# Performance work log

Hardware: AMD Instinct MI355X
Metric: run time of the kernel (lower is better)

## Reference

```python
import jax, jax.numpy as jnp
import numpy as np

B, T, C, H, S = 4, 1024, 768, 12, 64  # batch, seq, emb_dim, n_heads, head_size
FF = 4 * C          # 3072, ff_hidden_size (required by SwiGLU input dim)
HID = int(8 * C / 3)  # 2048, SwiGLU hidden
EPS = 1e-6


def _rope_tables(seq_len, dim):
    # theta = 10000 ** (-2 * arange(0, dim, 2) / dim)  (note extra factor 2 vs standard RoPE)
    theta = 10000.0 ** (-2.0 * jnp.arange(0, dim, 2, dtype=jnp.float32) / dim)
    freqs = jnp.arange(seq_len, dtype=jnp.float32)[:, None] * theta  # [T, dim/2]
    cos = jnp.repeat(jnp.cos(freqs), 2, axis=-1)  # [T, dim]
    sin = jnp.repeat(jnp.sin(freqs), 2, axis=-1)
    return cos, sin


def _rope(x, cos, sin):
    # x: [..., T, S]; rotate pairs: even' = -odd, odd' = even
    rot = jnp.stack([-x[..., 1::2], x[..., 0::2]], axis=-1).reshape(x.shape)
    return x * cos + rot * sin


def _rmsnorm(x, gamma):
    # global scalar RMS over the whole tensor (faithful to torch.mean with no dim)
    return x / jnp.sqrt(EPS + jnp.mean(x * x)) * gamma


def _block(x, Wq, Wk, Wv, Wo, g1, g2, W1, b1, Ww, bw, Wg, bg, Wd, bd, W2, b2):
    Tlen = x.shape[1]
    cos, sin = _rope_tables(Tlen, S)
    # --- multi-head attention on rms1(x) ---
    h = _rmsnorm(x, g1)
    q = jnp.einsum('btc,hcs->bhts', h, Wq)
    k = jnp.einsum('btc,hcs->bhts', h, Wk)
    v = jnp.einsum('btc,hcs->bhts', h, Wv)
    rq = _rope(q, cos, sin)
    rk = _rope(k, cos, sin)
    scores = jnp.einsum('bhts,bhks->bhtk', rq, rk) * (C ** -0.5)  # scale by emb_dim, faithful
    causal = jnp.tril(jnp.ones((Tlen, Tlen), dtype=bool))
    scores = jnp.where(causal, scores, -jnp.inf)
    probs = jax.nn.softmax(scores, axis=-1)
    attn = jnp.einsum('bhtk,bhks->bhts', probs, v)
    attn = attn.transpose(0, 2, 1, 3).reshape(x.shape[0], Tlen, C)  # concat heads
    out = x + attn @ Wo
    # --- feed forward on rms2(out) ---
    h2 = _rmsnorm(out, g2)
    u = h2 @ W1 + b1                      # [B,T,FF]
    wx = u @ Ww + bw                      # [B,T,HID]
    vx = u @ Wg + bg
    ff = (wx * (vx * jax.nn.sigmoid(vx))) @ Wd + bd  # [B,T,FF]
    ff = ff @ W2 + b2                     # [B,T,C]
    return out + ff


def setup_inputs() -> dict:
    key = jax.random.key(0)
    ks = jax.random.split(key, 17)
    sd = 0.02
    return {
        'x':  jax.random.normal(ks[0], (B, T, C), jnp.float32),
        'Wq': jax.random.normal(ks[1], (H, C, S), jnp.float32) * sd,
        'Wk': jax.random.normal(ks[2], (H, C, S), jnp.float32) * sd,
        'Wv': jax.random.normal(ks[3], (H, C, S), jnp.float32) * sd,
        'Wo': jax.random.normal(ks[4], (C, C), jnp.float32) * sd,
        'g1': jnp.ones((C,), jnp.float32),
        'g2': jnp.ones((C,), jnp.float32),
        'W1': jax.random.normal(ks[5], (C, FF), jnp.float32) * sd,
        'b1': jnp.zeros((FF,), jnp.float32),
        'Ww': jax.random.normal(ks[6], (FF, HID), jnp.float32) * sd,
        'bw': jnp.zeros((HID,), jnp.float32),
        'Wg': jax.random.normal(ks[7], (FF, HID), jnp.float32) * sd,
        'bg': jnp.zeros((HID,), jnp.float32),
        'Wd': jax.random.normal(ks[8], (HID, FF), jnp.float32) * sd,
        'bd': jnp.zeros((FF,), jnp.float32),
        'W2': jax.random.normal(ks[9], (FF, C), jnp.float32) * sd,
        'b2': jnp.zeros((C,), jnp.float32),
    }


def reference(x, Wq, Wk, Wv, Wo, g1, g2, W1, b1, Ww, bw, Wg, bg, Wd, bd, W2, b2):
    return _block(x, Wq, Wk, Wv, Wo, g1, g2, W1, b1, Ww, bw, Wg, bg, Wd, bd, W2, b2)
```

## Files before the change

kernel.cpp:

```cpp
#include <hip/hip_runtime.h>
#include <math.h>

#define BB   4
#define TT   1024
#define CC   768
#define HH   12
#define SS   64
#define FFD  3072
#define HIDD 2048
#define NTOK (BB*TT)
#define EPSR 1e-6f

typedef __attribute__((ext_vector_type(8))) short bf16x8;
typedef __attribute__((ext_vector_type(4))) float f32x4;

__device__ __forceinline__ unsigned short f2bf(float f) {
    unsigned u = __float_as_uint(f);
    return (unsigned short)((u + 0x7FFFu + ((u >> 16) & 1u)) >> 16);
}
__device__ __forceinline__ float bfl(unsigned u) { return __uint_as_float(u << 16); }
__device__ __forceinline__ float bfh(unsigned u) { return __uint_as_float(u & 0xFFFF0000u); }
__device__ __forceinline__ unsigned pk2(float a, float b) {
    return (unsigned)f2bf(a) | ((unsigned)f2bf(b) << 16);
}

__device__ __forceinline__ void gload_lds16(const unsigned short* g, unsigned short* l) {
    __builtin_amdgcn_global_load_lds(
        (const __attribute__((address_space(1))) unsigned int*)g,
        (__attribute__((address_space(3))) unsigned int*)l, 16, 0, 0);
}

__global__ void k_scale_gamma_b(const float* __restrict__ x, const float* __restrict__ g,
                                const float* __restrict__ part, unsigned short* __restrict__ h,
                                int n8, float invn, int npart) {
    __shared__ float sm[256];
    float s = 0.f;
    for (int i = threadIdx.x; i < npart; i += 256) s += part[i];
    sm[threadIdx.x] = s;
    __syncthreads();
    for (int off = 128; off > 0; off >>= 1) {
        if (threadIdx.x < off) sm[threadIdx.x] += sm[threadIdx.x + off];
        __syncthreads();
    }
    float sc = 1.0f / sqrtf(EPSR + sm[0] * invn);
    int i = blockIdx.x * blockDim.x + threadIdx.x;
    if (i >= n8) return;
    float4 v0 = ((const float4*)x)[2*i];
    float4 v1 = ((const float4*)x)[2*i+1];
    int c = (i * 8) % CC;
    float4 g0 = *(const float4*)(g + c);
    float4 g1v = *(const float4*)(g + c + 4);
    uint4 r;
    r.x = pk2(v0.x*sc*g0.x,  v0.y*sc*g0.y);
    r.y = pk2(v0.z*sc*g0.z,  v0.w*sc*g0.w);
    r.z = pk2(v1.x*sc*g1v.x, v1.y*sc*g1v.y);
    r.w = pk2(v1.z*sc*g1v.z, v1.w*sc*g1v.w);
    ((uint4*)h)[i] = r;
}

#define TQKV 1728
#define TWO  576
#define TW1  2304
#define TWW  6144
#define TWD  6144
#define TW2  2304
#define J0 (TQKV)
#define J1 (J0 + TWO)
#define J2 (J1 + TW1)
#define J3 (J2 + TWW)
#define J4 (J3 + TWW)
#define J5 (J4 + TWD)
#define J6 (J5 + TW2)
#define J7 (J6 + 16)
#define J8 (J7 + 128)
#define JSUM 1024
#define J9 (J8 + JSUM)

__device__ __forceinline__ void wT_tile(float (*tl)[33], const float* __restrict__ W,
                                        unsigned short* __restrict__ Wt,
                                        int K, int N, int t, int tx, int ty) {
    int nk = K >> 5;
    int k0 = (t % nk) * 32, n0 = (t / nk) * 32;
#pragma unroll
    for (int i = 0; i < 4; ++i)
        tl[ty + i*8][tx] = W[(size_t)(k0 + ty + i*8) * N + n0 + tx];
    __syncthreads();
#pragma unroll
    for (int i = 0; i < 4; ++i)
        Wt[(size_t)(n0 + ty + i*8) * K + k0 + tx] = f2bf(tl[tx][ty + i*8]);
}

__global__ void k_prep(const float* __restrict__ Wq, const float* __restrict__ Wk,
                       const float* __restrict__ Wv, const float* __restrict__ Wo,
                       const float* __restrict__ W1, const float* __restrict__ Ww,
                       const float* __restrict__ Wg, const float* __restrict__ Wd,
                       const float* __restrict__ W2, const float* __restrict__ bw,
                       const float* __restrict__ bg, const float* __restrict__ x,
                       unsigned short* __restrict__ wqkvT, unsigned short* __restrict__ WoT,
                       unsigned short* __restrict__ W1T, unsigned short* __restrict__ WcatT,
                       unsigned short* __restrict__ WdT, unsigned short* __restrict__ W2T,
                       float* __restrict__ bcat, float* __restrict__ tab,
                       float* __restrict__ part) {
    __shared__ float tl[32][33];
    const int bid = blockIdx.x;
    const int tx = threadIdx.x & 31, ty = threadIdx.x >> 5;
    if (bid < J0) {
        int t = bid;
        int c0 = (t % 24) * 32;
        int s0 = ((t / 24) & 1) * 32;
        int z = t / 48, sel = z / HH, h = z % HH;
        const float* W = (sel == 0 ? Wq : (sel == 1 ? Wk : Wv)) + (size_t)h * CC * SS;
#pragma unroll
        for (int i = 0; i < 4; ++i)
            tl[ty + i*8][tx] = W[(size_t)(c0 + ty + i*8) * SS + s0 + tx];
        __syncthreads();
#pragma unroll
        for (int i = 0; i < 4; ++i)
            wqkvT[(size_t)(sel*CC + h*SS + s0 + ty + i*8) * CC + c0 + tx] = f2bf(tl[tx][ty + i*8]);
    } else if (bid < J1) {
        wT_tile(tl, Wo, WoT, CC, CC, bid - J0, tx, ty);
    } else if (bid < J2) {
        wT_tile(tl, W1, W1T, CC, FFD, bid - J1, tx, ty);
    } else if (bid < J3) {
        wT_tile(tl, Ww, WcatT, FFD, HIDD, bid - J2, tx, ty);
    } else if (bid < J4) {
        wT_tile(tl, Wg, WcatT + (size_t)HIDD*FFD, FFD, HIDD, bid - J3, tx, ty);
    } else if (bid < J5) {
        wT_tile(tl, Wd, WdT, HIDD, FFD, bid - J4, tx, ty);
    } else if (bid < J6) {
        wT_tile(tl, W2, W2T, FFD, CC, bid - J5, tx, ty);
    } else if (bid < J7) {
        int i = (bid - J6) * 256 + threadIdx.x;
        bcat[i] = (i < HIDD) ? bw[i] : bg[i - HIDD];
    } else if (bid < J8) {
        int i = (bid - J7) * 256 + threadIdx.x;
        int t = i >> 5, j = i & 31;
        float th = expf(-(float)j * 0.5756462732485115f);
        float ang = (float)t * th;
        tab[2*i]   = cosf(ang);
        tab[2*i+1] = sinf(ang);
    } else {
        float* sm = &tl[0][0];
        const int pb = bid - J8;
        const int n4 = NTOK * CC / 4;
        float s = 0.f;
        int stride = JSUM * 256;
        for (int i = pb * 256 + threadIdx.x; i < n4; i += stride) {
            float4 v = ((const float4*)x)[i];
            s += v.x*v.x + v.y*v.y + v.z*v.z + v.w*v.w;
        }
        sm[threadIdx.x] = s;
        __syncthreads();
        for (int off = 128; off > 0; off >>= 1) {
            if (threadIdx.x < off) sm[threadIdx.x] += sm[threadIdx.x + off];
            __syncthreads();
        }
        if (threadIdx.x == 0) part[pb] = sm[0];
    }
}

__global__ void k_rope_vt(unsigned short* __restrict__ qkv, const float* __restrict__ tab,
                          unsigned short* __restrict__ vtg) {
    const int bid = blockIdx.x;
    if (bid < 6144) {
        int i = bid * 256 + threadIdx.x;
        int j  = i & 31;
        int h  = (i >> 5) % HH;
        int bt = i / (32 * HH);
        int t  = bt & (TT - 1);
        float cs = tab[(t*32 + j)*2];
        float sn = tab[(t*32 + j)*2 + 1];
        size_t base = (size_t)bt * (3*CC) + h * SS + 2*j;
        unsigned q = *(unsigned*)(qkv + base);
        float qe = bfl(q), qo = bfh(q);
        *(unsigned*)(qkv + base) = pk2(qe*cs - qo*sn, qo*cs + qe*sn);
        unsigned k = *(unsigned*)(qkv + base + CC);
        float ke = bfl(k), ko = bfh(k);
        *(unsigned*)(qkv + base + CC) = pk2(ke*cs - ko*sn, ko*cs + ke*sn);
    } else {
        int b2 = bid - 6144;
        int bh = b2 >> 3, ty = b2 & 7;
        int b = bh / HH, h = bh % HH;
        int d = threadIdx.x & 63, tq = threadIdx.x >> 6;
        int t0 = ty * 128 + tq * 32;
        const unsigned short* src = qkv + (size_t)(b*TT + t0)*(3*CC) + 2*CC + h*SS + d;
        unsigned v[16];
#pragma unroll
        for (int e = 0; e < 16; ++e) {
            unsigned lo = src[(size_t)(2*e)*(3*CC)];
            unsigned hi = src[(size_t)(2*e+1)*(3*CC)];
            v[e] = (lo & 0xFFFFu) | (hi << 16);
        }
        uint4* dst = (uint4*)(vtg + ((size_t)bh*64 + d)*TT + t0);
#pragma unroll
        for (int q = 0; q < 4; ++q)
            dst[q] = make_uint4(v[q*4], v[q*4+1], v[q*4+2], v[q*4+3]);
    }
}

template<bool BIAS, bool RES, bool OUTB, bool SSQ>
__global__ __launch_bounds__(256) void k_gemm_bf16(
    const unsigned short* __restrict__ A, const unsigned short* __restrict__ Bt,
    const float* __restrict__ bias, const float* __restrict__ res,
    void* __restrict__ Cv, int M, int N, int K, float* __restrict__ ssq_part)
{
    __shared__ unsigned short As[2][128*32];
    __shared__ unsigned short Bs[2][128*32];
    __shared__ float smr[256];
    const int tid  = threadIdx.x;
    const int w    = tid >> 6, lane = tid & 63;
    const int wr   = w >> 1,  wc   = w & 1;
    const int row0 = blockIdx.y * 128, col0 = blockIdx.x * 128;

    f32x4 acc[4][4];
#pragma unroll
    for (int m = 0; m < 4; ++m)
#pragma unroll
        for (int n = 0; n < 4; ++n) acc[m][n] = (f32x4){0.f, 0.f, 0.f, 0.f};

    const int lr4 = lane >> 2;
    const int scb = lane & 3;

    auto stage = [&](int t, int buf) {
#pragma unroll
        for (int i = 0; i < 2; ++i) {
            int lr = w * 32 + i * 16 + lr4;
            int cbs = scb ^ ((lr >> 1) & 3);
            const unsigned short* ga = A + (size_t)(row0 + lr) * K + t * 32 + cbs * 8;
            gload_lds16(ga, &As[buf][(w * 32 + i * 16) * 32]);
            const unsigned short* gb = Bt + (size_t)(col0 + lr) * K + t * 32 + cbs * 8;
            gload_lds16(gb, &Bs[buf][(w * 32 + i * 16) * 32]);
        }
    };

    const int nt = K / 32;
    stage(0, 0);
    int cur = 0;
    const int fr = lane & 15, fq = lane >> 4;
    for (int t = 0; t < nt; ++t) {
        __syncthreads();
        if (t + 1 < nt) stage(t + 1, cur ^ 1);
        bf16x8 af[4], bf[4];
#pragma unroll
        for (int m = 0; m < 4; ++m) {
            int ra = wr * 64 + m * 16 + fr;
            af[m] = *(const bf16x8*)&As[cur][ra * 32 + (fq ^ ((ra >> 1) & 3)) * 8];
            int rb = wc * 64 + m * 16 + fr;
            bf[m] = *(const bf16x8*)&Bs[cur][rb * 32 + (fq ^ ((rb >> 1) & 3)) * 8];
        }
#pragma unroll
        for (int m = 0; m < 4; ++m)
#pragma unroll
            for (int n = 0; n < 4; ++n)
                acc[m][n] = __builtin_amdgcn_mfma_f32_16x16x32_bf16(af[m], bf[n], acc[m][n], 0, 0, 0);
        cur ^= 1;
    }

    float ssq = 0.f;
#pragma unroll
    for (int m = 0; m < 4; ++m) {
#pragma unroll
        for (int n = 0; n < 4; ++n) {
            int col = col0 + wc * 64 + n * 16 + fr;
            float bv = BIAS ? bias[col] : 0.f;
#pragma unroll
            for (int j = 0; j < 4; ++j) {
                int row = row0 + wr * 64 + m * 16 + fq * 4 + j;
                size_t off = (size_t)row * N + col;
                float v = acc[m][n][j] + bv;
                if (RES) v += res[off];
                if (OUTB) ((unsigned short*)Cv)[off] = f2bf(v);
                else      ((float*)Cv)[off] = v;
                if (SSQ) ssq += v * v;
            }
        }
    }
    if (SSQ) {
        smr[tid] = ssq;
        __syncthreads();
        for (int off = 128; off > 0; off >>= 1) {
            if (tid < off) smr[tid] += smr[tid + off];
            __syncthreads();
        }
        if (tid == 0) ssq_part[blockIdx.y * gridDim.x + blockIdx.x] = smr[0];
    }
}

#define INTERVAL(s_, RA, RB, NA, NB, DOSTAGE, DONEXT, LGKM, GATE)                 \
    {                                                                             \
        if (DONEXT) {                                                             \
            const int nx_ = ((s_) + 1) & 3;                                       \
            _Pragma("unroll")                                                     \
            for (int m = 0; m < 8; ++m)                                           \
                NA[m] = *(const bf16x8*)&ringA[nx_][offA[m]];                     \
            _Pragma("unroll")                                                     \
            for (int n = 0; n < 4; ++n)                                           \
                NB[n] = *(const bf16x8*)&ringB[nx_][offB[n]];                     \
        }                                                                         \
        if (DOSTAGE) { stageA((s_) + 3); stageB((s_) + 3); }                      \
        __builtin_amdgcn_sched_barrier(0);                                        \
        asm volatile("s_waitcnt " LGKM ::: "memory");                             \
        __builtin_amdgcn_sched_barrier(0);                                        \
        __builtin_amdgcn_s_setprio(1);                                            \
        _Pragma("unroll")                                                         \
        for (int m = 0; m < 8; ++m)                                               \
            _Pragma("unroll")                                                     \
            for (int n = 0; n < 4; ++n)                                           \
                acc[m][n] = __builtin_amdgcn_mfma_f32_16x16x32_bf16(              \
                    RA[m], RB[n], acc[m][n], 0, 0, 0);                            \
        __builtin_amdgcn_s_setprio(0);                                            \
        asm volatile("s_waitcnt " GATE ::: "memory");                             \
        __builtin_amdgcn_sched_barrier(0);                                        \
        __builtin_amdgcn_s_barrier();                                             \
    }

template<bool BIAS>
__global__ __launch_bounds__(512, 2) void k_gemm256(
    const unsigned short* __restrict__ A, const unsigned short* __restrict__ Bt,
    const float* __restrict__ bias, unsigned short* __restrict__ C,
    int M, int N, int K)
{
    __shared__ __align__(16) unsigned short ringA[4][256*32];
    __shared__ __align__(16) unsigned short ringB[4][256*32];
    const int tid = threadIdx.x;
    const int w = tid >> 6, lane = tid & 63;
    const int wm = w >> 2, wn = w & 3;
    const int fr = lane & 15, fq = lane >> 4;

    const int nwg = gridDim.x * gridDim.y;
    const int bid = blockIdx.y * gridDim.x + blockIdx.x;
    const int cpx = nwg >> 3;
    const int sbid = (bid & 7) * cpx + (bid >> 3);
    const int row0 = (sbid / gridDim.x) * 256;
    const int col0 = (sbid % gridDim.x) * 256;

    f32x4 acc[8][4];
#pragma unroll
    for (int m = 0; m < 8; ++m)
#pragma unroll
        for (int n = 0; n < 4; ++n) acc[m][n] = (f32x4){0.f, 0.f, 0.f, 0.f};

    const int c0 = tid, c1 = 512 + tid;
    const int r0 = c0 >> 2, p0 = ((c0 & 3) ^ ((r0 >> 1) & 3)) * 8;
    const int r1 = c1 >> 2, p1 = ((c1 & 3) ^ ((r1 >> 1) & 3)) * 8;
    const unsigned short* aS0 = A  + (size_t)(row0 + r0) * K + p0;
    const unsigned short* aS1 = A  + (size_t)(row0 + r1) * K + p1;
    const unsigned short* bS0 = Bt + (size_t)(col0 + r0) * K + p0;
    const unsigned short* bS1 = Bt + (size_t)(col0 + r1) * K + p1;
    const int dL = w * 512;
    auto stageA = [&](int t) {
        const int st = t & 3;
        const int kb = t * 32;
        gload_lds16(aS0 + kb, &ringA[st][dL]);
        gload_lds16(aS1 + kb, &ringA[st][4096 + dL]);
    };
    auto stageB = [&](int t) {
        const int st = t & 3;
        const int kb = t * 32;
        gload_lds16(bS0 + kb, &ringB[st][dL]);
        gload_lds16(bS1 + kb, &ringB[st][4096 + dL]);
    };

    int offA[8], offB[4];
#pragma unroll
    for (int m = 0; m < 8; ++m) {
        int ra = wm*128 + m*16 + fr;
        offA[m] = ra*32 + (fq ^ ((ra >> 1) & 3))*8;
    }
#pragma unroll
    for (int n = 0; n < 4; ++n) {
        int rb = wn*64 + n*16 + fr;
        offB[n] = rb*32 + (fq ^ ((rb >> 1) & 3))*8;
    }

    const int S = K >> 5;
    stageA(0); stageB(0); stageA(1); stageB(1); stageA(2); stageB(2);
    asm volatile("s_waitcnt vmcnt(4)" ::: "memory");
    __builtin_amdgcn_s_barrier();

    bf16x8 A0[8], B0[4], A1[8], B1[4];
#pragma unroll
    for (int m = 0; m < 8; ++m) A0[m] = *(const bf16x8*)&ringA[0][offA[m]];
#pragma unroll
    for (int n = 0; n < 4; ++n) B0[n] = *(const bf16x8*)&ringB[0][offB[n]];

    int s = 0;
    for (; s < S - 4; s += 2) {
        INTERVAL(s,   A0, B0, A1, B1, true, true, "lgkmcnt(12)", "vmcnt(4)");
        INTERVAL(s+1, A1, B1, A0, B0, true, true, "lgkmcnt(12)", "vmcnt(4)");
    }
    INTERVAL(S-4, A0, B0, A1, B1, true,  true,  "lgkmcnt(12)", "vmcnt(4)");
    INTERVAL(S-3, A1, B1, A0, B0, false, true,  "lgkmcnt(12)", "vmcnt(0)");
    INTERVAL(S-2, A0, B0, A1, B1, false, true,  "lgkmcnt(12)", "vmcnt(0)");
    INTERVAL(S-1, A1, B1, A0, B0, false, false, "lgkmcnt(0)",  "vmcnt(0)");

#pragma unroll
    for (int m = 0; m < 8; ++m) {
#pragma unroll
        for (int n = 0; n < 4; ++n) {
            int col = col0 + wn*64 + n*16 + fr;
            float bvb = BIAS ? bias[col] : 0.f;
#pragma unroll
            for (int j = 0; j < 4; ++j) {
                int row = row0 + wm*128 + m*16 + fq*4 + j;
                C[(size_t)row * N + col] = f2bf(acc[m][n][j] + bvb);
            }
        }
    }
}

__global__ __launch_bounds__(256) void k_attn_mfma(
    const unsigned short* __restrict__ qkv, const unsigned short* __restrict__ vtg,
    unsigned short* __restrict__ attn)
{
    __shared__ __align__(16) unsigned short Ks[2][64*64];
    __shared__ __align__(16) unsigned short Vs[2][64*64];
    __shared__ __align__(16) unsigned short Ps[4][16*72];
    const int tid = threadIdx.x;
    const int w = tid >> 6, lane = tid & 63;
    const int fr = lane & 15, fq = lane >> 4;
    const int bh = blockIdx.x, b = bh / HH, h = bh % HH;
    const int qb = blockIdx.y * 64;
    const int nkt = qb / 64 + 1;
    const float scale = 0.03608439182435161f;

    bf16x8 qf[2];
    {
        const unsigned short* qp = qkv + (size_t)(b*TT + qb + w*16 + fr)*(3*CC) + h*SS + fq*8;
        qf[0] = *(const bf16x8*)qp;
        qf[1] = *(const bf16x8*)(qp + 32);
    }

    auto stage = [&](int kt, int buf) {
        const unsigned short* kbase = qkv + (size_t)(b*TT + kt*64)*(3*CC) + CC + h*SS;
        const unsigned short* vbase = vtg + ((size_t)bh*64)*TT + kt*64;
#pragma unroll
        for (int p = 0; p < 2; ++p) {
            int s = p*256 + tid;
            int row = s >> 3;
            int blk = (s & 7) ^ (row & 7);
            gload_lds16(kbase + (size_t)row*(3*CC) + blk*8, &Ks[buf][(p*256 + w*64)*8]);
            gload_lds16(vbase + (size_t)row*TT + blk*8,     &Vs[buf][(p*256 + w*64)*8]);
        }
    };

    float m[4] = {-INFINITY, -INFINITY, -INFINITY, -INFINITY};
    float l[4] = {0.f, 0.f, 0.f, 0.f};
    f32x4 oacc[4];
#pragma unroll
    for (int n = 0; n < 4; ++n) oacc[n] = (f32x4){0.f, 0.f, 0.f, 0.f};

    stage(0, 0);
    int cur = 0;
    for (int kt = 0; kt < nkt; ++kt) {
        __syncthreads();
        if (kt + 1 < nkt) stage(kt + 1, cur ^ 1);

        f32x4 sacc[4];
#pragma unroll
        for (int n = 0; n < 4; ++n) sacc[n] = (f32x4){0.f, 0.f, 0.f, 0.f};
#pragma unroll
        for (int ks = 0; ks < 2; ++ks) {
#pragma unroll
            for (int n = 0; n < 4; ++n) {
                int row = n*16 + fr;
                bf16x8 kf = *(const bf16x8*)&Ks[cur][row*64 + ((ks*4 + fq) ^ (row & 7))*8];
                sacc[n] = __builtin_amdgcn_mfma_f32_16x16x32_bf16(qf[ks], kf, sacc[n], 0, 0, 0);
            }
        }

        float sv[4][4];
        const bool lastt = (kt == nkt - 1);
        const int qloc = w*16 + fq*4;
#pragma unroll
        for (int n = 0; n < 4; ++n) {
            int kloc = n*16 + fr;
#pragma unroll
            for (int j = 0; j < 4; ++j) {
                float vv = sacc[n][j] * scale;
                if (lastt && kloc > qloc + j) vv = -INFINITY;
                sv[j][n] = vv;
            }
        }
        float mx[4], ls[4];
#pragma unroll
        for (int j = 0; j < 4; ++j)
            mx[j] = fmaxf(fmaxf(sv[j][0], sv[j][1]), fmaxf(sv[j][2], sv[j][3]));
#pragma unroll
        for (int d = 1; d < 16; d <<= 1)
#pragma unroll
            for (int j = 0; j < 4; ++j) mx[j] = fmaxf(mx[j], __shfl_xor(mx[j], d));
        float corr[4];
#pragma unroll
        for (int j = 0; j < 4; ++j) {
            float nm = fmaxf(m[j], mx[j]);
            corr[j] = __expf(m[j] - nm);
            m[j] = nm;
        }
#pragma unroll
        for (int j = 0; j < 4; ++j) {
            float s0 = 0.f;
#pragma unroll
            for (int n = 0; n < 4; ++n) {
                float p = __expf(sv[j][n] - m[j]);
                sv[j][n] = p;
                s0 += p;
            }
            ls[j] = s0;
        }
#pragma unroll
        for (int d = 1; d < 16; d <<= 1)
#pragma unroll
            for (int j = 0; j < 4; ++j) ls[j] += __shfl_xor(ls[j], d);
#pragma unroll
        for (int j = 0; j < 4; ++j) l[j] = l[j]*corr[j] + ls[j];
#pragma unroll
        for (int n = 0; n < 4; ++n)
#pragma unroll
            for (int j = 0; j < 4; ++j) oacc[n][j] *= corr[j];

#pragma unroll
        for (int j = 0; j < 4; ++j)
#pragma unroll
            for (int n = 0; n < 4; ++n)
                Ps[w][(fq*4 + j)*72 + n*16 + fr] = f2bf(sv[j][n]);

#pragma unroll
        for (int ks = 0; ks < 2; ++ks) {
            bf16x8 pf = *(const bf16x8*)&Ps[w][fr*72 + ks*32 + fq*8];
#pragma unroll
            for (int n = 0; n < 4; ++n) {
                int row = n*16 + fr;
                bf16x8 vf = *(const bf16x8*)&Vs[cur][row*64 + ((ks*4 + fq) ^ (row & 7))*8];
                oacc[n] = __builtin_amdgcn_mfma_f32_16x16x32_bf16(pf, vf, oacc[n], 0, 0, 0);
            }
        }
        cur ^= 1;
    }

    float inv[4];
#pragma unroll
    for (int j = 0; j < 4; ++j) inv[j] = 1.0f / l[j];
#pragma unroll
    for (int n = 0; n < 4; ++n)
#pragma unroll
        for (int j = 0; j < 4; ++j) {
            size_t off = (size_t)(b*TT + qb + w*16 + fq*4 + j)*CC + h*SS + n*16 + fr;
            attn[off] = f2bf(oacc[n][j] * inv[j]);
        }
}

__global__ void k_swiglu_uv(const unsigned short* __restrict__ uv,
                            unsigned short* __restrict__ sw, int n8) {
    int i = blockIdx.x * blockDim.x + threadIdx.x;
    if (i >= n8) return;
    int r = i >> 8;
    int c8 = (i & 255) * 8;
    uint4 wv = *(const uint4*)(uv + (size_t)r * (2*HIDD) + c8);
    uint4 vv = *(const uint4*)(uv + (size_t)r * (2*HIDD) + HIDD + c8);
    uint4 rr;
    float w0, w1, v0, v1;
    w0 = bfl(wv.x); w1 = bfh(wv.x); v0 = bfl(vv.x); v1 = bfh(vv.x);
    rr.x = pk2(w0*v0/(1.f+__expf(-v0)), w1*v1/(1.f+__expf(-v1)));
    w0 = bfl(wv.y); w1 = bfh(wv.y); v0 = bfl(vv.y); v1 = bfh(vv.y);
    rr.y = pk2(w0*v0/(1.f+__expf(-v0)), w1*v1/(1.f+__expf(-v1)));
    w0 = bfl(wv.z); w1 = bfh(wv.z); v0 = bfl(vv.z); v1 = bfh(vv.z);
    rr.z = pk2(w0*v0/(1.f+__expf(-v0)), w1*v1/(1.f+__expf(-v1)));
    w0 = bfl(wv.w); w1 = bfh(wv.w); v0 = bfl(vv.w); v1 = bfh(vv.w);
    rr.w = pk2(w0*v0/(1.f+__expf(-v0)), w1*v1/(1.f+__expf(-v1)));
    *(uint4*)(sw + (size_t)r * HIDD + c8) = rr;
}

extern "C" void kernel_launch(void* const* d_in, const int* in_sizes, int n_in,
                              void* d_out, int out_size, void* d_ws, size_t ws_size,
                              hipStream_t stream)
{
    const float* x  = (const float*)d_in[0];
    const float* Wq = (const float*)d_in[1];
    const float* Wk = (const float*)d_in[2];
    const float* Wv = (const float*)d_in[3];
    const float* Wo = (const float*)d_in[4];
    const float* g1 = (const float*)d_in[5];
    const float* g2 = (const float*)d_in[6];
    const float* W1 = (const float*)d_in[7];
    const float* b1 = (const float*)d_in[8];
    const float* Ww = (const float*)d_in[9];
    const float* bw = (const float*)d_in[10];
    const float* Wg = (const float*)d_in[11];
    const float* bg = (const float*)d_in[12];
    const float* Wd = (const float*)d_in[13];
    const float* bd = (const float*)d_in[14];
    const float* W2 = (const float*)d_in[15];
    const float* b2 = (const float*)d_in[16];
    float* out = (float*)d_out;

    char* p = (char*)d_ws;
    auto alloc = [&](size_t bytes) { char* r = p; p += (bytes + 255) & ~(size_t)255; return r; };

    float*          part   = (float*)alloc(4096);
    float*          tab    = (float*)alloc((size_t)TT*32*2*4);
    float*          bcat   = (float*)alloc((size_t)2*HIDD*4);
    unsigned short* hb     = (unsigned short*)alloc((size_t)NTOK*CC*2);
    unsigned short* wqkvT  = (unsigned short*)alloc((size_t)3*CC*CC*2);
    unsigned short* qkvb   = (unsigned short*)alloc((size_t)NTOK*3*CC*2);
    unsigned short* vtg    = (unsigned short*)alloc((size_t)BB*HH*SS*TT*2);
    unsigned short* attnb  = (unsigned short*)alloc((size_t)NTOK*CC*2);
    unsigned short* WoT    = (unsigned short*)alloc((size_t)CC*CC*2);
    unsigned short* W1T    = (unsigned short*)alloc((size_t)FFD*CC*2);
    unsigned short* ub     = (unsigned short*)alloc((size_t)NTOK*FFD*2);
    unsigned short* WcatT  = (unsigned short*)alloc((size_t)2*HIDD*FFD*2);
    unsigned short* uvcat  = (unsigned short*)alloc((size_t)NTOK*2*HIDD*2);
    unsigned short* swb    = (unsigned short*)alloc((size_t)NTOK*HIDD*2);
    unsigned short* WdT    = (unsigned short*)alloc((size_t)FFD*HIDD*2);
    unsigned short* W2T    = (unsigned short*)alloc((size_t)CC*FFD*2);

    const int n = NTOK * CC;

    k_prep<<<J9, 256, 0, stream>>>(Wq, Wk, Wv, Wo, W1, Ww, Wg, Wd, W2, bw, bg, x,
                                   wqkvT, WoT, W1T, WcatT, WdT, W2T, bcat, tab, part);

    k_scale_gamma_b<<<(n/8)/256, 256, 0, stream>>>(x, g1, part, hb, n/8,
                                                   1.0f/(float)n, JSUM);

    k_gemm256<false><<<dim3(3*CC/256, NTOK/256), 512, 0, stream>>>(
        hb, wqkvT, nullptr, qkvb, NTOK, 3*CC, CC);
    k_rope_vt<<<6144 + 384, 256, 0, stream>>>(qkvb, tab, vtg);

    k_attn_mfma<<<dim3(BB*HH, TT/64), 256, 0, stream>>>(qkvb, vtg, attnb);

    k_gemm_bf16<false,true,false,true><<<dim3(CC/128, NTOK/128), 256, 0, stream>>>(
        attnb, WoT, nullptr, x, out, NTOK, CC, CC, part);

    k_scale_gamma_b<<<(n/8)/256, 256, 0, stream>>>(out, g2, part, hb, n/8,
                                                   1.0f/(float)n, (CC/128)*(NTOK/128));

    k_gemm256<true><<<dim3(FFD/256, NTOK/256), 512, 0, stream>>>(
        hb, W1T, b1, ub, NTOK, FFD, CC);
    k_gemm256<true><<<dim3(2*HIDD/256, NTOK/256), 512, 0, stream>>>(
        ub, WcatT, bcat, uvcat, NTOK, 2*HIDD, FFD);
    k_swiglu_uv<<<(NTOK*HIDD/8)/256, 256, 0, stream>>>(uvcat, swb, NTOK*HIDD/8);
    k_gemm256<true><<<dim3(FFD/256, NTOK/256), 512, 0, stream>>>(
        swb, WdT, bd, ub, NTOK, FFD, HIDD);
    k_gemm_bf16<true,true,false,false><<<dim3(CC/128, NTOK/128), 256, 0, stream>>>(
        ub, W2T, b2, out, out, NTOK, CC, FFD, nullptr);
}
```

Baseline: 391.8 us.

## Fuse SwiGLU into Ww/Wg GEMM epilogue via interleaved weights; simplify GEMM pipeline

```diff
diff --git a/kernel.cpp b/kernel.cpp
--- a/kernel.cpp
+++ b/kernel.cpp
@@ -88,6 +88,20 @@
 #pragma unroll
     for (int i = 0; i < 4; ++i)
         Wt[(size_t)(n0 + ty + i*8) * K + k0 + tx] = f2bf(tl[tx][ty + i*8]);
+}
+
+__device__ __forceinline__ void wT_tile_il(float (*tl)[33], const float* __restrict__ W,
+                                           unsigned short* __restrict__ Wt,
+                                           int K, int N, int t, int tx, int ty, int ofs) {
+    int nk = K >> 5;
+    int k0 = (t % nk) * 32, n0 = (t / nk) * 32;
+#pragma unroll
+    for (int i = 0; i < 4; ++i)
+        tl[ty + i*8][tx] = W[(size_t)(k0 + ty + i*8) * N + n0 + tx];
+    __syncthreads();
+#pragma unroll
+    for (int i = 0; i < 4; ++i)
+        Wt[(size_t)(2*(n0 + ty + i*8) + ofs) * K + k0 + tx] = f2bf(tl[tx][ty + i*8]);
 }
 
 __global__ void k_prep(const float* __restrict__ Wq, const float* __restrict__ Wk,
@@ -122,16 +136,16 @@
     } else if (bid < J2) {
         wT_tile(tl, W1, W1T, CC, FFD, bid - J1, tx, ty);
     } else if (bid < J3) {
-        wT_tile(tl, Ww, WcatT, FFD, HIDD, bid - J2, tx, ty);
+        wT_tile_il(tl, Ww, WcatT, FFD, HIDD, bid - J2, tx, ty, 0);
     } else if (bid < J4) {
-        wT_tile(tl, Wg, WcatT + (size_t)HIDD*FFD, FFD, HIDD, bid - J3, tx, ty);
+        wT_tile_il(tl, Wg, WcatT, FFD, HIDD, bid - J3, tx, ty, 1);
     } else if (bid < J5) {
         wT_tile(tl, Wd, WdT, HIDD, FFD, bid - J4, tx, ty);
     } else if (bid < J6) {
         wT_tile(tl, W2, W2T, FFD, CC, bid - J5, tx, ty);
     } else if (bid < J7) {
         int i = (bid - J6) * 256 + threadIdx.x;
-        bcat[i] = (i < HIDD) ? bw[i] : bg[i - HIDD];
+        bcat[i] = (i & 1) ? bg[i >> 1] : bw[i >> 1];
     } else if (bid < J8) {
         int i = (bid - J7) * 256 + threadIdx.x;
         int t = i >> 5, j = i & 31;
@@ -286,20 +300,20 @@
     }
 }
 
-#define INTERVAL(s_, RA, RB, NA, NB, DOSTAGE, DONEXT, LGKM, GATE)                 \
+#define GSTEP(s_, DOSTAGE, GATE)                                                  \
     {                                                                             \
-        if (DONEXT) {                                                             \
-            const int nx_ = ((s_) + 1) & 3;                                       \
-            _Pragma("unroll")                                                     \
-            for (int m = 0; m < 8; ++m)                                           \
-                NA[m] = *(const bf16x8*)&ringA[nx_][offA[m]];                     \
-            _Pragma("unroll")                                                     \
-            for (int n = 0; n < 4; ++n)                                           \
-                NB[n] = *(const bf16x8*)&ringB[nx_][offB[n]];                     \
-        }                                                                         \
+        const int st_ = (s_) & 3;                                                 \
+        const unsigned short* pa_ = &ringA[st_][0];                               \
+        const unsigned short* pb_ = &ringB[st_][0];                               \
+        bf16x8 af[8], bv[4];                                                      \
+        _Pragma("unroll")                                                         \
+        for (int m = 0; m < 8; ++m)                                               \
+            af[m] = *(const bf16x8*)&pa_[offA[m]];                                \
+        _Pragma("unroll")                                                         \
+        for (int n = 0; n < 4; ++n)                                               \
+            bv[n] = *(const bf16x8*)&pb_[offB[n]];                                \
         if (DOSTAGE) { stageA((s_) + 3); stageB((s_) + 3); }                      \
-        __builtin_amdgcn_sched_barrier(0);                                        \
-        asm volatile("s_waitcnt " LGKM ::: "memory");                             \
+        asm volatile("s_waitcnt lgkmcnt(0)" ::: "memory");                        \
         __builtin_amdgcn_sched_barrier(0);                                        \
         __builtin_amdgcn_s_setprio(1);                                            \
         _Pragma("unroll")                                                         \
@@ -307,14 +321,14 @@
             _Pragma("unroll")                                                     \
             for (int n = 0; n < 4; ++n)                                           \
                 acc[m][n] = __builtin_amdgcn_mfma_f32_16x16x32_bf16(              \
-                    RA[m], RB[n], acc[m][n], 0, 0, 0);                            \
+                    af[m], bv[n], acc[m][n], 0, 0, 0);                            \
         __builtin_amdgcn_s_setprio(0);                                            \
         asm volatile("s_waitcnt " GATE ::: "memory");                             \
         __builtin_amdgcn_sched_barrier(0);                                        \
         __builtin_amdgcn_s_barrier();                                             \
     }
 
-template<bool BIAS>
+template<bool BIAS, bool SWIGLU>
 __global__ __launch_bounds__(512, 2) void k_gemm256(
     const unsigned short* __restrict__ A, const unsigned short* __restrict__ Bt,
     const float* __restrict__ bias, unsigned short* __restrict__ C,
@@ -375,24 +389,13 @@
 
     const int S = K >> 5;
     stageA(0); stageB(0); stageA(1); stageB(1); stageA(2); stageB(2);
-    asm volatile("s_waitcnt vmcnt(4)" ::: "memory");
+    asm volatile("s_waitcnt vmcnt(8)" ::: "memory");
     __builtin_amdgcn_s_barrier();
-
-    bf16x8 A0[8], B0[4], A1[8], B1[4];
-#pragma unroll
-    for (int m = 0; m < 8; ++m) A0[m] = *(const bf16x8*)&ringA[0][offA[m]];
-#pragma unroll
-    for (int n = 0; n < 4; ++n) B0[n] = *(const bf16x8*)&ringB[0][offB[n]];
-
     int s = 0;
-    for (; s < S - 4; s += 2) {
-        INTERVAL(s,   A0, B0, A1, B1, true, true, "lgkmcnt(12)", "vmcnt(4)");
-        INTERVAL(s+1, A1, B1, A0, B0, true, true, "lgkmcnt(12)", "vmcnt(4)");
-    }
-    INTERVAL(S-4, A0, B0, A1, B1, true,  true,  "lgkmcnt(12)", "vmcnt(4)");
-    INTERVAL(S-3, A1, B1, A0, B0, false, true,  "lgkmcnt(12)", "vmcnt(0)");
-    INTERVAL(S-2, A0, B0, A1, B1, false, true,  "lgkmcnt(12)", "vmcnt(0)");
-    INTERVAL(S-1, A1, B1, A0, B0, false, false, "lgkmcnt(0)",  "vmcnt(0)");
+    for (; s < S - 3; ++s) GSTEP(s, true, "vmcnt(8)");
+    GSTEP(s, false, "vmcnt(4)"); ++s;
+    GSTEP(s, false, "vmcnt(0)"); ++s;
+    GSTEP(s, false, "vmcnt(0)");
 
 #pragma unroll
     for (int m = 0; m < 8; ++m) {
@@ -403,7 +406,16 @@
 #pragma unroll
             for (int j = 0; j < 4; ++j) {
                 int row = row0 + wm*128 + m*16 + fq*4 + j;
-                C[(size_t)row * N + col] = f2bf(acc[m][n][j] + bvb);
+                float v = acc[m][n][j] + bvb;
+                if (SWIGLU) {
+                    float pv = __shfl_xor(v, 1);
+                    if (!(fr & 1)) {
+                        float sw = v * pv / (1.f + __expf(-pv));
+                        C[(size_t)row * (N >> 1) + (col >> 1)] = f2bf(sw);
+                    }
+                } else {
+                    C[(size_t)row * N + col] = f2bf(v);
+                }
             }
         }
     }
@@ -548,27 +560,6 @@
             size_t off = (size_t)(b*TT + qb + w*16 + fq*4 + j)*CC + h*SS + n*16 + fr;
             attn[off] = f2bf(oacc[n][j] * inv[j]);
         }
-}
-
-__global__ void k_swiglu_uv(const unsigned short* __restrict__ uv,
-                            unsigned short* __restrict__ sw, int n8) {
-    int i = blockIdx.x * blockDim.x + threadIdx.x;
-    if (i >= n8) return;
-    int r = i >> 8;
-    int c8 = (i & 255) * 8;
-    uint4 wv = *(const uint4*)(uv + (size_t)r * (2*HIDD) + c8);
-    uint4 vv = *(const uint4*)(uv + (size_t)r * (2*HIDD) + HIDD + c8);
-    uint4 rr;
-    float w0, w1, v0, v1;
-    w0 = bfl(wv.x); w1 = bfh(wv.x); v0 = bfl(vv.x); v1 = bfh(vv.x);
-    rr.x = pk2(w0*v0/(1.f+__expf(-v0)), w1*v1/(1.f+__expf(-v1)));
-    w0 = bfl(wv.y); w1 = bfh(wv.y); v0 = bfl(vv.y); v1 = bfh(vv.y);
-    rr.y = pk2(w0*v0/(1.f+__expf(-v0)), w1*v1/(1.f+__expf(-v1)));
-    w0 = bfl(wv.z); w1 = bfh(wv.z); v0 = bfl(vv.z); v1 = bfh(vv.z);
-    rr.z = pk2(w0*v0/(1.f+__expf(-v0)), w1*v1/(1.f+__expf(-v1)));
-    w0 = bfl(wv.w); w1 = bfh(wv.w); v0 = bfl(vv.w); v1 = bfh(vv.w);
-    rr.w = pk2(w0*v0/(1.f+__expf(-v0)), w1*v1/(1.f+__expf(-v1)));
-    *(uint4*)(sw + (size_t)r * HIDD + c8) = rr;
 }
 
 extern "C" void kernel_launch(void* const* d_in, const int* in_sizes, int n_in,
@@ -609,7 +600,6 @@
     unsigned short* W1T    = (unsigned short*)alloc((size_t)FFD*CC*2);
     unsigned short* ub     = (unsigned short*)alloc((size_t)NTOK*FFD*2);
     unsigned short* WcatT  = (unsigned short*)alloc((size_t)2*HIDD*FFD*2);
-    unsigned short* uvcat  = (unsigned short*)alloc((size_t)NTOK*2*HIDD*2);
     unsigned short* swb    = (unsigned short*)alloc((size_t)NTOK*HIDD*2);
     unsigned short* WdT    = (unsigned short*)alloc((size_t)FFD*HIDD*2);
     unsigned short* W2T    = (unsigned short*)alloc((size_t)CC*FFD*2);
@@ -622,7 +612,7 @@
     k_scale_gamma_b<<<(n/8)/256, 256, 0, stream>>>(x, g1, part, hb, n/8,
                                                    1.0f/(float)n, JSUM);
 
-    k_gemm256<false><<<dim3(3*CC/256, NTOK/256), 512, 0, stream>>>(
+    k_gemm256<false,false><<<dim3(3*CC/256, NTOK/256), 512, 0, stream>>>(
         hb, wqkvT, nullptr, qkvb, NTOK, 3*CC, CC);
     k_rope_vt<<<6144 + 384, 256, 0, stream>>>(qkvb, tab, vtg);
 
@@ -634,12 +624,11 @@
     k_scale_gamma_b<<<(n/8)/256, 256, 0, stream>>>(out, g2, part, hb, n/8,
                                                    1.0f/(float)n, (CC/128)*(NTOK/128));
 
-    k_gemm256<true><<<dim3(FFD/256, NTOK/256), 512, 0, stream>>>(
+    k_gemm256<true,false><<<dim3(FFD/256, NTOK/256), 512, 0, stream>>>(
         hb, W1T, b1, ub, NTOK, FFD, CC);
-    k_gemm256<true><<<dim3(2*HIDD/256, NTOK/256), 512, 0, stream>>>(
-        ub, WcatT, bcat, uvcat, NTOK, 2*HIDD, FFD);
-    k_swiglu_uv<<<(NTOK*HIDD/8)/256, 256, 0, stream>>>(uvcat, swb, NTOK*HIDD/8);
-    k_gemm256<true><<<dim3(FFD/256, NTOK/256), 512, 0, stream>>>(
+    k_gemm256<true,true><<<dim3(2*HIDD/256, NTOK/256), 512, 0, stream>>>(
+        ub, WcatT, bcat, swb, NTOK, 2*HIDD, FFD);
+    k_gemm256<true,false><<<dim3(FFD/256, NTOK/256), 512, 0, stream>>>(
         swb, WdT, bd, ub, NTOK, FFD, HIDD);
     k_gemm_bf16<true,true,false,false><<<dim3(CC/128, NTOK/128), 256, 0, stream>>>(
         ub, W2T, b2, out, out, NTOK, CC, FFD, nullptr);
```

After: 386.7 us. Within noise of the previous version (-1.3%).
